# Optimization experiments

Hardware: AMD Instinct MI355X
Metric: run time of the kernel (lower is better)

The kernel has to match this reference:

```python
import jax, jax.numpy as jnp
import numpy as np

ALPHA = 0.2          # LeakyReLU negative slope
NEG_INF = -9e15      # mask value used by the original module


def setup_inputs() -> dict:
    key = jax.random.key(0)
    k1, k2, k3, k4 = jax.random.split(key, 4)
    N, F_IN, F_OUT = 8192, 512, 256
    inp = jax.random.normal(k1, (N, F_IN), dtype=jnp.float32)
    W = jax.random.normal(k2, (F_IN, F_OUT), dtype=jnp.float32) * (1.414 / np.sqrt(F_IN))
    a = jax.random.normal(k3, (2 * F_OUT, 1), dtype=jnp.float32) * (1.414 / np.sqrt(F_OUT))
    adj = jax.random.randint(k4, (N, N), 0, 2, dtype=jnp.int32)
    return {"input": inp, "W": W, "a": a, "adj": adj}


def reference(input, W, a, adj):
    # h: [N, F_out]
    h = input @ W
    F_out = h.shape[1]
    # Original builds a_input[i,j] = concat(h_i, h_j) then matmuls with a.
    # Equivalent: e_ij = leakyrelu(h_i . a[:F] + h_j . a[F:]) without the O(N^2 * 2F) tensor.
    a1 = a[:F_out, 0]   # [F_out]
    a2 = a[F_out:, 0]   # [F_out]
    s1 = h @ a1         # [N]
    s2 = h @ a2         # [N]
    e = jax.nn.leaky_relu(s1[:, None] + s2[None, :], negative_slope=ALPHA)  # [N, N]
    attention = jax.nn.softmax(jnp.where(adj > 0, e, NEG_INF), axis=1)       # [N, N]
    return attention @ h  # [N, F_out]
```

## Files before the change

### kernel.cpp

```cpp
#include <hip/hip_runtime.h>


typedef __attribute__((ext_vector_type(8))) short bf16x8;
typedef __attribute__((ext_vector_type(4))) float fx4;
typedef __attribute__((ext_vector_type(4))) int ix4;
typedef __attribute__((ext_vector_type(2))) unsigned int ux2;

#define NN 8192
#define FIN 512
#define FOUT 256
#define PS 136
#define AROWS 64

__device__ __forceinline__ unsigned short f2bf(float f) {
    unsigned int x = __float_as_uint(f);
    x += 0x7fffu + ((x >> 16) & 1u);
    return (unsigned short)(x >> 16);
}
__device__ __forceinline__ bf16x8 pack8(fx4 a, fx4 b) {
    bf16x8 r;
    r[0] = (short)f2bf(a[0]); r[1] = (short)f2bf(a[1]);
    r[2] = (short)f2bf(a[2]); r[3] = (short)f2bf(a[3]);
    r[4] = (short)f2bf(b[0]); r[5] = (short)f2bf(b[1]);
    r[6] = (short)f2bf(b[2]); r[7] = (short)f2bf(b[3]);
    return r;
}

__global__ void wt_kernel(const float* __restrict__ W,
                          unsigned short* __restrict__ WTt) {
    const int c = threadIdx.x;
    const int k = blockIdx.x;
    WTt[((size_t)(k >> 5) * 256 + c) * 32 + (k & 31)] = f2bf(W[k * FOUT + c]);
}

__global__ __launch_bounds__(256) void prep_kernel(
    const float* __restrict__ X,
    const unsigned short* __restrict__ WTt,
    const float* __restrict__ A,
    unsigned short* __restrict__ hTt,
    float* __restrict__ s1, float* __restrict__ s2)
{
    __shared__ float s1sh[4][16], s2sh[4][16];
    const int tid = threadIdx.x;

    const int w = tid >> 6, l = tid & 63, q = l >> 4, lr = l & 15;
    const int r0 = blockIdx.x * 16;
    const int cbase = w * 64;
    fx4 acc[4] = {};

    for (int kb = 0; kb < FIN; kb += 32) {
        const float* xp = X + (size_t)(r0 + lr) * FIN + kb + q * 8;
        bf16x8 a0 = pack8(*(const fx4*)xp, *(const fx4*)(xp + 4));
#pragma unroll
        for (int tc = 0; tc < 4; ++tc) {
            bf16x8 b = *(const bf16x8*)(WTt + ((size_t)(kb >> 5) * 256 + cbase + tc * 16 + lr) * 32 + q * 8);
            acc[tc] = __builtin_amdgcn_mfma_f32_16x16x32_bf16(a0, b, acc[tc], 0, 0, 0);
        }
    }

    const int jb = r0 >> 5, jo = (r0 & 31) + q * 4;
#pragma unroll
    for (int tc = 0; tc < 4; ++tc) {
        const int c = cbase + tc * 16 + lr;
        ux2 hp;
        hp.x = (unsigned)f2bf(acc[tc][0]) | ((unsigned)f2bf(acc[tc][1]) << 16);
        hp.y = (unsigned)f2bf(acc[tc][2]) | ((unsigned)f2bf(acc[tc][3]) << 16);
        *(ux2*)(hTt + ((size_t)jb * 256 + c) * 32 + jo) = hp;
    }

    float p1[4] = {}, p2[4] = {};
#pragma unroll
    for (int tc = 0; tc < 4; ++tc) {
        const int c = cbase + tc * 16 + lr;
        const float a1v = A[c], a2v = A[FOUT + c];
#pragma unroll
        for (int r = 0; r < 4; ++r) {
            p1[r] += acc[tc][r] * a1v;
            p2[r] += acc[tc][r] * a2v;
        }
    }
#pragma unroll
    for (int r = 0; r < 4; ++r) {
#pragma unroll
        for (int off = 1; off < 16; off <<= 1) {
            p1[r] += __shfl_xor(p1[r], off);
            p2[r] += __shfl_xor(p2[r], off);
        }
        if (lr == 0) { s1sh[w][q * 4 + r] = p1[r]; s2sh[w][q * 4 + r] = p2[r]; }
    }
    __syncthreads();
    if (tid < 16) {
        s1[r0 + tid] = s1sh[0][tid] + s1sh[1][tid] + s1sh[2][tid] + s1sh[3][tid];
        s2[r0 + tid] = s2sh[0][tid] + s2sh[1][tid] + s2sh[2][tid] + s2sh[3][tid];
    }
}

__global__ __launch_bounds__(512, 2) void attn_kernel(
    const int* __restrict__ adj,
    const unsigned short* __restrict__ hTt,
    const float* __restrict__ s1,
    const float* __restrict__ s2,
    float* __restrict__ num,
    float* __restrict__ den)
{
    __shared__ unsigned short P[2][AROWS * PS];
    const int tid = threadIdx.x;
    const int rg = blockIdx.x >> 1;
    const int kh = blockIdx.x & 1;
    const int r0 = rg * AROWS;
    const int khB = kh * 32;

    const int prow = tid >> 3;
    const int pq = tid & 7;
    const float s1v = s1[r0 + prow];
    const int* arow = adj + (size_t)(r0 + prow) * NN + (size_t)kh * 4096 + pq * 8;
    float denp = 0.f;

    const int w = tid >> 6, l = tid & 63, q = l >> 4, lr = l & 15;
    const int cbase = w * 32;
    fx4 acc[4][2] = {};

    struct LSet { ix4 v0, v1; fx4 s2a, s2b; };
    LSet SA, SB;
    bf16x8 B0[4][2], B1[4][2];

    auto loadS = [&](int s, int kq, LSet& L) {
        const int* ap = arow + s * 128 + kq * 64;
        L.v0 = __builtin_nontemporal_load((const ix4*)ap);
        L.v1 = __builtin_nontemporal_load((const ix4*)(ap + 4));
        const float* sp = s2 + (khB + s) * 128 + kq * 64 + pq * 8;
        L.s2a = *(const fx4*)sp;
        L.s2b = *(const fx4*)(sp + 4);
    };
    auto calcP = [&](int b, int kq, const LSet& L) {
        bf16x8 pv;
#pragma unroll
        for (int j = 0; j < 8; ++j) {
            const int aj = (j < 4) ? L.v0[j] : L.v1[j - 4];
            const float s2j = (j < 4) ? L.s2a[j] : L.s2b[j - 4];
            float t = s1v + s2j;
            float e = fmaxf(t, 0.2f * t);
            e = fminf(e, 30.f);
            const float p = (aj != 0) ? __expf(e) : 0.f;
            denp += p;
            pv[j] = (short)f2bf(p);
        }
        *(bf16x8*)(&P[b][prow * PS + kq * 64 + pq * 8]) = pv;
    };
    auto loadB = [&](int s, bf16x8 (&B)[4][2]) {
        const int kt = khB + s;
#pragma unroll
        for (int ks = 0; ks < 4; ++ks)
#pragma unroll
            for (int tc = 0; tc < 2; ++tc)
                B[ks][tc] = *(const bf16x8*)(hTt + ((size_t)(kt * 4 + ks) * 256 + cbase + tc * 16 + lr) * 32 + q * 8);
    };

    auto ldsBarrier = [&]() {
        asm volatile("s_waitcnt lgkmcnt(0)" ::: "memory");
        __builtin_amdgcn_s_barrier();
    };

    const int ITERS = 32;

    loadS(0, 0, SA); loadS(0, 1, SB);
    calcP(0, 0, SA); calcP(0, 1, SB);
    loadS(1, 0, SA); loadS(1, 1, SB);
    loadB(0, B0);
    ldsBarrier();

    auto body = [&](int it, bf16x8 (&Bc)[4][2], bf16x8 (&Bn)[4][2]) {
        if (it + 1 < ITERS) loadB(it + 1, Bn);
        const unsigned short* Pb = P[it & 1];
#pragma unroll
        for (int rg4 = 0; rg4 < 4; ++rg4) {
            bf16x8 af[4];
#pragma unroll
            for (int ks = 0; ks < 4; ++ks)
                af[ks] = *(const bf16x8*)(Pb + (rg4 * 16 + lr) * PS + ks * 32 + q * 8);
            __builtin_amdgcn_s_setprio(1);
#pragma unroll
            for (int ks = 0; ks < 4; ++ks)
#pragma unroll
                for (int tc = 0; tc < 2; ++tc)
                    acc[rg4][tc] = __builtin_amdgcn_mfma_f32_16x16x32_bf16(af[ks], Bc[ks][tc], acc[rg4][tc], 0, 0, 0);
            __builtin_amdgcn_s_setprio(0);
        }
        if (it + 1 < ITERS) {
            calcP((it + 1) & 1, 0, SA);
            calcP((it + 1) & 1, 1, SB);
        }
        if (it + 2 < ITERS) {
            loadS(it + 2, 0, SA);
            loadS(it + 2, 1, SB);
        }
        ldsBarrier();
    };

    for (int it = 0; it < ITERS; it += 2) {
        body(it, B0, B1);
        body(it + 1, B1, B0);
    }

    float v = denp;
    v += __shfl_xor(v, 1);
    v += __shfl_xor(v, 2);
    v += __shfl_xor(v, 4);
    if (pq == 0) den[(size_t)kh * NN + r0 + prow] = v;

    float* nb = num + (size_t)kh * NN * FOUT;
#pragma unroll
    for (int rg4 = 0; rg4 < 4; ++rg4)
#pragma unroll
        for (int r = 0; r < 4; ++r) {
            const int row = rg4 * 16 + q * 4 + r;
#pragma unroll
            for (int tc = 0; tc < 2; ++tc)
                nb[(size_t)(r0 + row) * FOUT + cbase + tc * 16 + lr] = acc[rg4][tc][r];
        }
}

__global__ __launch_bounds__(512) void combine_kernel(
    const float* __restrict__ num, const float* __restrict__ den,
    float* __restrict__ out)
{
    const int idx = blockIdx.x * 512 + threadIdx.x;
    const int r = idx >> 6;
    const fx4 a = *(const fx4*)(num + (size_t)idx * 4);
    const fx4 b = *(const fx4*)(num + (size_t)NN * FOUT + (size_t)idx * 4);
    const float dinv = 1.0f / fmaxf(den[r] + den[NN + r], 1e-30f);
    fx4 o;
#pragma unroll
    for (int j = 0; j < 4; ++j) o[j] = (a[j] + b[j]) * dinv;
    *(fx4*)(out + (size_t)idx * 4) = o;
}

extern "C" void kernel_launch(void* const* d_in, const int* in_sizes, int n_in,
                              void* d_out, int out_size, void* d_ws, size_t ws_size,
                              hipStream_t stream) {
    const float *X = nullptr, *W = nullptr, *A = nullptr;
    const int* adj = nullptr;
    for (int i = 0; i < n_in; ++i) {
        switch (in_sizes[i]) {
            case NN * FIN:   X = (const float*)d_in[i]; break;
            case FIN * FOUT: W = (const float*)d_in[i]; break;
            case 2 * FOUT:   A = (const float*)d_in[i]; break;
            case NN * NN:    adj = (const int*)d_in[i]; break;
        }
    }
    if (!X) X = (const float*)d_in[0];
    if (!W) W = (const float*)d_in[1];
    if (!A) A = (const float*)d_in[2];
    if (!adj) adj = (const int*)d_in[3];
    float* out = (float*)d_out;

    char* ws = (char*)d_ws;
    float* s1 = (float*)ws;
    float* s2 = (float*)(ws + 32768);
    unsigned short* WTt = (unsigned short*)(ws + 98304);
    unsigned short* hTt = (unsigned short*)(ws + 360448);
    float* num = (float*)(ws + 8388608);
    float* den = (float*)(ws + 25165824);

    wt_kernel<<<512, 256, 0, stream>>>(W, WTt);
    prep_kernel<<<512, 256, 0, stream>>>(X, WTt, A, hTt, s1, s2);
    attn_kernel<<<(NN / AROWS) * 2, 512, 0, stream>>>(adj, hTt, s1, s2, num, den);
    combine_kernel<<<1024, 512, 0, stream>>>(num, den, out);
}
```

Before: 413.3 us.

## Use 128-row tiles with 4-way K split and single-buffered P

The attention kernel now processes 128 rows per block and splits the key dimension four ways instead of two, so each B fragment loaded from hTt is reused across twice as many rows. The double-buffered P/prefetch pipeline is replaced by a simpler loop: load the adjacency ints, compute P into one LDS buffer, synchronize, run the MFMAs, synchronize again. The combine kernel now sums four partial numerators and denominators, which doubles partial-result traffic. Dropping the overlap and doubling the accumulator registers may hurt latency hiding and occupancy.

```diff
diff --git a/kernel.cpp b/kernel.cpp
--- a/kernel.cpp
+++ b/kernel.cpp
@@ -10,7 +10,7 @@
 #define FIN 512
 #define FOUT 256
 #define PS 136
-#define AROWS 64
+#define AROWS 128
 
 __device__ __forceinline__ unsigned short f2bf(float f) {
     unsigned int x = __float_as_uint(f);
@@ -103,120 +103,112 @@
     float* __restrict__ num,
     float* __restrict__ den)
 {
-    __shared__ unsigned short P[2][AROWS * PS];
+    __shared__ unsigned short P[AROWS * PS];
+
     const int tid = threadIdx.x;
-    const int rg = blockIdx.x >> 1;
-    const int kh = blockIdx.x & 1;
+    const int rg = blockIdx.x >> 2;
+    const int kq = blockIdx.x & 3;
     const int r0 = rg * AROWS;
-    const int khB = kh * 32;
-
-    const int prow = tid >> 3;
-    const int pq = tid & 7;
+    const int kb0 = kq * 16;
+
+    const int prow = tid >> 2;
+    const int pq = tid & 3;
     const float s1v = s1[r0 + prow];
-    const int* arow = adj + (size_t)(r0 + prow) * NN + (size_t)kh * 4096 + pq * 8;
+    const int* arow = adj + (size_t)(r0 + prow) * NN + kq * 2048 + pq * 8;
     float denp = 0.f;
 
     const int w = tid >> 6, l = tid & 63, q = l >> 4, lr = l & 15;
     const int cbase = w * 32;
-    fx4 acc[4][2] = {};
-
-    struct LSet { ix4 v0, v1; fx4 s2a, s2b; };
-    LSet SA, SB;
-    bf16x8 B0[4][2], B1[4][2];
-
-    auto loadS = [&](int s, int kq, LSet& L) {
-        const int* ap = arow + s * 128 + kq * 64;
-        L.v0 = __builtin_nontemporal_load((const ix4*)ap);
-        L.v1 = __builtin_nontemporal_load((const ix4*)(ap + 4));
-        const float* sp = s2 + (khB + s) * 128 + kq * 64 + pq * 8;
-        L.s2a = *(const fx4*)sp;
-        L.s2b = *(const fx4*)(sp + 4);
-    };
-    auto calcP = [&](int b, int kq, const LSet& L) {
-        bf16x8 pv;
-#pragma unroll
-        for (int j = 0; j < 8; ++j) {
-            const int aj = (j < 4) ? L.v0[j] : L.v1[j - 4];
-            const float s2j = (j < 4) ? L.s2a[j] : L.s2b[j - 4];
-            float t = s1v + s2j;
-            float e = fmaxf(t, 0.2f * t);
-            e = fminf(e, 30.f);
-            const float p = (aj != 0) ? __expf(e) : 0.f;
-            denp += p;
-            pv[j] = (short)f2bf(p);
-        }
-        *(bf16x8*)(&P[b][prow * PS + kq * 64 + pq * 8]) = pv;
-    };
-    auto loadB = [&](int s, bf16x8 (&B)[4][2]) {
-        const int kt = khB + s;
+    fx4 acc[8][2] = {};
+
+    ix4 av[8];
+    bf16x8 B[4][2];
+
+    auto loadA = [&](int it) {
+        const int* ap = arow + it * 128;
+#pragma unroll
+        for (int j8 = 0; j8 < 4; ++j8) {
+            av[2 * j8]     = __builtin_nontemporal_load((const ix4*)(ap + j8 * 32));
+            av[2 * j8 + 1] = __builtin_nontemporal_load((const ix4*)(ap + j8 * 32 + 4));
+        }
+    };
+    auto loadB = [&](int it) {
+        const int kt = kb0 + it;
 #pragma unroll
         for (int ks = 0; ks < 4; ++ks)
 #pragma unroll
             for (int tc = 0; tc < 2; ++tc)
                 B[ks][tc] = *(const bf16x8*)(hTt + ((size_t)(kt * 4 + ks) * 256 + cbase + tc * 16 + lr) * 32 + q * 8);
     };
-
+    auto phaseA = [&](int it) {
+        fx4 s2v[8];
+        const float* sp = s2 + (kb0 + it) * 128 + pq * 8;
+#pragma unroll
+        for (int j8 = 0; j8 < 4; ++j8) {
+            s2v[2 * j8]     = *(const fx4*)(sp + j8 * 32);
+            s2v[2 * j8 + 1] = *(const fx4*)(sp + j8 * 32 + 4);
+        }
+#pragma unroll
+        for (int j8 = 0; j8 < 4; ++j8) {
+            bf16x8 pv;
+#pragma unroll
+            for (int j = 0; j < 8; ++j) {
+                const int aj = (j < 4) ? av[2 * j8][j] : av[2 * j8 + 1][j - 4];
+                const float s2j = (j < 4) ? s2v[2 * j8][j] : s2v[2 * j8 + 1][j - 4];
+                float t = s1v + s2j;
+                float e = fmaxf(t, 0.2f * t);
+                e = fminf(e, 30.f);
+                const float p = (aj != 0) ? __expf(e) : 0.f;
+                denp += p;
+                pv[j] = (short)f2bf(p);
+            }
+            *(bf16x8*)(&P[prow * PS + j8 * 32 + pq * 8]) = pv;
+        }
+    };
     auto ldsBarrier = [&]() {
         asm volatile("s_waitcnt lgkmcnt(0)" ::: "memory");
         __builtin_amdgcn_s_barrier();
     };
 
-    const int ITERS = 32;
-
-    loadS(0, 0, SA); loadS(0, 1, SB);
-    calcP(0, 0, SA); calcP(0, 1, SB);
-    loadS(1, 0, SA); loadS(1, 1, SB);
-    loadB(0, B0);
-    ldsBarrier();
-
-    auto body = [&](int it, bf16x8 (&Bc)[4][2], bf16x8 (&Bn)[4][2]) {
-        if (it + 1 < ITERS) loadB(it + 1, Bn);
-        const unsigned short* Pb = P[it & 1];
-#pragma unroll
-        for (int rg4 = 0; rg4 < 4; ++rg4) {
+    const int ITERS = 16;
+
+    loadA(0);
+    for (int it = 0; it < ITERS; ++it) {
+        loadB(it);
+        phaseA(it);
+        if (it + 1 < ITERS) loadA(it + 1);
+        ldsBarrier();
+#pragma unroll
+        for (int rg8 = 0; rg8 < 8; ++rg8) {
             bf16x8 af[4];
 #pragma unroll
             for (int ks = 0; ks < 4; ++ks)
-                af[ks] = *(const bf16x8*)(Pb + (rg4 * 16 + lr) * PS + ks * 32 + q * 8);
+                af[ks] = *(const bf16x8*)(&P[(rg8 * 16 + lr) * PS + ks * 32 + q * 8]);
             __builtin_amdgcn_s_setprio(1);
 #pragma unroll
             for (int ks = 0; ks < 4; ++ks)
 #pragma unroll
                 for (int tc = 0; tc < 2; ++tc)
-                    acc[rg4][tc] = __builtin_amdgcn_mfma_f32_16x16x32_bf16(af[ks], Bc[ks][tc], acc[rg4][tc], 0, 0, 0);
+                    acc[rg8][tc] = __builtin_amdgcn_mfma_f32_16x16x32_bf16(af[ks], B[ks][tc], acc[rg8][tc], 0, 0, 0);
             __builtin_amdgcn_s_setprio(0);
         }
-        if (it + 1 < ITERS) {
-            calcP((it + 1) & 1, 0, SA);
-            calcP((it + 1) & 1, 1, SB);
-        }
-        if (it + 2 < ITERS) {
-            loadS(it + 2, 0, SA);
-            loadS(it + 2, 1, SB);
-        }
         ldsBarrier();
-    };
-
-    for (int it = 0; it < ITERS; it += 2) {
-        body(it, B0, B1);
-        body(it + 1, B1, B0);
     }
 
     float v = denp;
     v += __shfl_xor(v, 1);
     v += __shfl_xor(v, 2);
-    v += __shfl_xor(v, 4);
-    if (pq == 0) den[(size_t)kh * NN + r0 + prow] = v;
-
-    float* nb = num + (size_t)kh * NN * FOUT;
-#pragma unroll
-    for (int rg4 = 0; rg4 < 4; ++rg4)
+    if (pq == 0) den[(size_t)kq * NN + r0 + prow] = v;
+
+    float* nb = num + (size_t)kq * NN * FOUT;
+#pragma unroll
+    for (int rg8 = 0; rg8 < 8; ++rg8)
 #pragma unroll
         for (int r = 0; r < 4; ++r) {
-            const int row = rg4 * 16 + q * 4 + r;
+            const int row = rg8 * 16 + q * 4 + r;
 #pragma unroll
             for (int tc = 0; tc < 2; ++tc)
-                nb[(size_t)(r0 + row) * FOUT + cbase + tc * 16 + lr] = acc[rg4][tc][r];
+                nb[(size_t)(r0 + row) * FOUT + cbase + tc * 16 + lr] = acc[rg8][tc][r];
         }
 }
 
@@ -224,14 +216,18 @@
     const float* __restrict__ num, const float* __restrict__ den,
     float* __restrict__ out)
 {
+    const size_t NF = (size_t)NN * FOUT;
     const int idx = blockIdx.x * 512 + threadIdx.x;
     const int r = idx >> 6;
     const fx4 a = *(const fx4*)(num + (size_t)idx * 4);
-    const fx4 b = *(const fx4*)(num + (size_t)NN * FOUT + (size_t)idx * 4);
-    const float dinv = 1.0f / fmaxf(den[r] + den[NN + r], 1e-30f);
+    const fx4 b = *(const fx4*)(num + NF + (size_t)idx * 4);
+    const fx4 c = *(const fx4*)(num + 2 * NF + (size_t)idx * 4);
+    const fx4 d = *(const fx4*)(num + 3 * NF + (size_t)idx * 4);
+    const float dt = den[r] + den[NN + r] + den[2 * NN + r] + den[3 * NN + r];
+    const float dinv = 1.0f / fmaxf(dt, 1e-30f);
     fx4 o;
 #pragma unroll
-    for (int j = 0; j < 4; ++j) o[j] = (a[j] + b[j]) * dinv;
+    for (int j = 0; j < 4; ++j) o[j] = (a[j] + b[j] + c[j] + d[j]) * dinv;
     *(fx4*)(out + (size_t)idx * 4) = o;
 }
 
@@ -260,10 +256,10 @@
     unsigned short* WTt = (unsigned short*)(ws + 98304);
     unsigned short* hTt = (unsigned short*)(ws + 360448);
     float* num = (float*)(ws + 8388608);
-    float* den = (float*)(ws + 25165824);
+    float* den = (float*)(ws + 41943040);
 
     wt_kernel<<<512, 256, 0, stream>>>(W, WTt);
     prep_kernel<<<512, 256, 0, stream>>>(X, WTt, A, hTt, s1, s2);
-    attn_kernel<<<(NN / AROWS) * 2, 512, 0, stream>>>(adj, hTt, s1, s2, num, den);
+    attn_kernel<<<(NN / AROWS) * 4, 512, 0, stream>>>(adj, hTt, s1, s2, num, den);
     combine_kernel<<<1024, 512, 0, stream>>>(num, den, out);
 }
```

Result: no change. 409.2 us (-1.0%).
